# Kernel optimization log

Measured on AMD Instinct MI355X. Metric: run time of the kernel, lower is better.

Reference implementation:

```python
import jax, jax.numpy as jnp
import numpy as np

B, S, E, H, L, D, G, V = 32, 256, 300, 256, 4000, 256, 512, 50000
LIN1, LIN2 = 512, 256  # linear_size


def _glorot(key, shape):
    fan_in, fan_out = shape[-1], shape[-2] if len(shape) > 1 else shape[-1]
    std = np.sqrt(2.0 / (fan_in + fan_out))
    return jax.random.normal(key, shape, dtype=jnp.float32) * std


def setup_inputs() -> dict:
    key = jax.random.key(0)
    ks = jax.random.split(key, 20)
    tokens = jax.random.randint(ks[0], (B, S), 1, V)  # avoid padding_idx=0
    emb_table = jax.random.normal(ks[1], (V, E), dtype=jnp.float32) * 0.1
    emb_table = emb_table.at[0].set(0.0)  # padding row
    # bidirectional LSTM (1 layer), torch gate order i,f,g,o
    w_ih_f = _glorot(ks[2], (4 * H, E));  w_hh_f = _glorot(ks[3], (4 * H, H))
    b_f = jnp.zeros((4 * H,), jnp.float32)
    w_ih_b = _glorot(ks[4], (4 * H, E));  w_hh_b = _glorot(ks[5], (4 * H, H))
    b_b = jnp.zeros((4 * H,), jnp.float32)
    # MLAttention: Linear(2H -> L, bias=False)
    attn_w = _glorot(ks[6], (L, 2 * H))
    # label graph branch
    label_emb = _glorot(ks[7], (L, D))
    adj_raw = (jax.random.uniform(ks[8], (L, L)) < 0.004).astype(jnp.float32)
    adj_raw = adj_raw + jnp.eye(L, dtype=jnp.float32)
    deg = jnp.sum(adj_raw, axis=1, keepdims=True)
    adj = adj_raw / deg  # row-normalized dense adjacency [L, L]
    gcn_w = _glorot(ks[9], (D, G));  gcn_b = jnp.zeros((G,), jnp.float32)
    # MLLinear([2H+G, 512, 256], 1)
    w1 = _glorot(ks[10], (2 * H + G, LIN1));  b1 = jnp.zeros((LIN1,), jnp.float32)
    w2 = _glorot(ks[11], (LIN1, LIN2));       b2 = jnp.zeros((LIN2,), jnp.float32)
    w_out = _glorot(ks[12], (LIN2, 1));       b_out = jnp.zeros((1,), jnp.float32)
    return dict(tokens=tokens, emb_table=emb_table,
                w_ih_f=w_ih_f, w_hh_f=w_hh_f, b_f=b_f,
                w_ih_b=w_ih_b, w_hh_b=w_hh_b, b_b=b_b,
                attn_w=attn_w, label_emb=label_emb, adj=adj,
                gcn_w=gcn_w, gcn_b=gcn_b,
                w1=w1, b1=b1, w2=w2, b2=b2, w_out=w_out, b_out=b_out)


def _lstm_dir(x_gates, w_hh, reverse):
    # x_gates: [B, S, 4H] precomputed input projections (+bias)
    def step(carry, xt):
        h, c = carry
        gates = xt + h @ w_hh.T
        i, f, g, o = jnp.split(gates, 4, axis=-1)
        c = jax.nn.sigmoid(f) * c + jax.nn.sigmoid(i) * jnp.tanh(g)
        h = jax.nn.sigmoid(o) * jnp.tanh(c)
        return (h, c), h
    b = x_gates.shape[0]
    init = (jnp.zeros((b, H), x_gates.dtype), jnp.zeros((b, H), x_gates.dtype))
    _, hs = jax.lax.scan(step, init, jnp.swapaxes(x_gates, 0, 1), reverse=reverse)
    return jnp.swapaxes(hs, 0, 1)  # [B, S, H]


def reference(tokens, emb_table, w_ih_f, w_hh_f, b_f, w_ih_b, w_hh_b, b_b,
              attn_w, label_emb, adj, gcn_w, gcn_b,
              w1, b1, w2, b2, w_out, b_out):
    masks = tokens != 0  # [B, S]
    emb_out = emb_table[tokens]  # [B, S, E]
    # bidirectional LSTM -> [B, S, 2H]
    gates_f = jnp.einsum('bse,ge->bsg', emb_out, w_ih_f) + b_f
    gates_b = jnp.einsum('bse,ge->bsg', emb_out, w_ih_b) + b_b
    rnn_out = jnp.concatenate([_lstm_dir(gates_f, w_hh_f, False),
                               _lstm_dir(gates_b, w_hh_b, True)], axis=-1)
    # MLAttention: per-label attention over sequence
    scores = jnp.einsum('bsh,lh->bls', rnn_out, attn_w)  # [B, L, S]
    scores = jnp.where(masks[:, None, :], scores, jnp.float32(-1e9))
    attn = jax.nn.softmax(scores, axis=-1)
    attn_out = jnp.einsum('bls,bsh->blh', attn, rnn_out)  # [B, L, 2H]
    # GCN over label graph: relu(A @ (X W) + b), single layer [D -> G]
    gcn_out = jax.nn.relu(adj @ (label_emb @ gcn_w) + gcn_b)  # [L, G]
    gcn_out = jnp.broadcast_to(gcn_out[None], (attn_out.shape[0], L, G))
    # concat fusion + MLLinear([2H+G, 512, 256], 1)
    x = jnp.concatenate([attn_out, gcn_out], axis=-1)  # [B, L, 2H+G]
    x = jax.nn.relu(x @ w1 + b1)
    x = jax.nn.relu(x @ w2 + b2)
    out = jnp.squeeze(x @ w_out + b_out, -1)  # [B, L]
    return out
```

## Files before the change

### kernel.cpp

```cpp
#include <hip/hip_runtime.h>
#include <hip/hip_bf16.h>
#include <math.h>


typedef __attribute__((ext_vector_type(8))) short bfrag;
typedef __attribute__((ext_vector_type(4))) float ffrag;

__device__ __forceinline__ ushort f2bf(float x) {
    union { float f; unsigned u; } c; c.f = x;
    const unsigned r = c.u + 0x7fffu + ((c.u >> 16) & 1u);
    return (ushort)(r >> 16);
}
__device__ __forceinline__ float bf2f(ushort h) {
    union { unsigned u; float f; } c; c.u = (unsigned)h << 16;
    return c.f;
}

template<bool BIAS, bool ADDROW, bool RELU, bool OUTF, bool OUTS, bool OUTDOT>
__global__ __launch_bounds__(256) void mgemm_k(
    const ushort* __restrict__ A, const ushort* __restrict__ B,
    float* __restrict__ Cf, ushort* __restrict__ Cs,
    int M, int N, int K, int lda, int ldb, int ldc, int ldcs,
    long abs_, long bbs_, long cbs_, long csbs_,
    const float* __restrict__ bias,
    const float* __restrict__ addrow, int addmod, int ldadd,
    const float* __restrict__ dotw, float* __restrict__ pd)
{
    const int tid = threadIdx.x;
    const int ln = tid & 63;
    const int wv = tid >> 6;
    const int wm = wv >> 1, wn = wv & 1;
    const int n0 = blockIdx.x * 128;
    const int m0 = blockIdx.y * 128;
    const int z = blockIdx.z;
    A += (size_t)z * abs_;
    B += (size_t)z * bbs_;

    __shared__ ushort Ah[128 * 40], Al[128 * 40], Bh[128 * 40], Bl[128 * 40];

    ffrag acc[4][4];
#pragma unroll
    for (int i = 0; i < 4; ++i)
#pragma unroll
        for (int j = 0; j < 4; ++j) acc[i][j] = ffrag{0.f, 0.f, 0.f, 0.f};

    const int sr = tid >> 1;
    const int sk = (tid & 1) * 16;
    const int am = min(m0 + sr, M - 1);
    const int bn = n0 + sr;
    const int fr = ln & 15;
    const int fk = (ln >> 4) * 8;

    const ushort* arow = A + (size_t)am * lda + sk;
    const ushort* brow = B + (size_t)bn * ldb + sk;

    bfrag ah0, ah1, al0, al1, bh0, bh1, bl0, bl1;
    {
        const ushort* ap = arow;
        const ushort* bp = brow;
        ah0 = *(const bfrag*)ap;       ah1 = *(const bfrag*)(ap + 8);
        al0 = *(const bfrag*)(ap + K); al1 = *(const bfrag*)(ap + K + 8);
        bh0 = *(const bfrag*)bp;       bh1 = *(const bfrag*)(bp + 8);
        bl0 = *(const bfrag*)(bp + K); bl1 = *(const bfrag*)(bp + K + 8);
    }

    for (int k0 = 0; k0 < K; k0 += 32) {
        __syncthreads();
        *(bfrag*)&Ah[sr * 40 + sk] = ah0;  *(bfrag*)&Ah[sr * 40 + sk + 8] = ah1;
        *(bfrag*)&Al[sr * 40 + sk] = al0;  *(bfrag*)&Al[sr * 40 + sk + 8] = al1;
        *(bfrag*)&Bh[sr * 40 + sk] = bh0;  *(bfrag*)&Bh[sr * 40 + sk + 8] = bh1;
        *(bfrag*)&Bl[sr * 40 + sk] = bl0;  *(bfrag*)&Bl[sr * 40 + sk + 8] = bl1;
        __syncthreads();
        if (k0 + 32 < K) {
            const ushort* ap = arow + k0 + 32;
            const ushort* bp = brow + k0 + 32;
            ah0 = *(const bfrag*)ap;       ah1 = *(const bfrag*)(ap + 8);
            al0 = *(const bfrag*)(ap + K); al1 = *(const bfrag*)(ap + K + 8);
            bh0 = *(const bfrag*)bp;       bh1 = *(const bfrag*)(bp + 8);
            bl0 = *(const bfrag*)(bp + K); bl1 = *(const bfrag*)(bp + K + 8);
        }
        bfrag afh[4], afl[4];
#pragma unroll
        for (int i = 0; i < 4; ++i) {
            const int ar = (wm * 64 + i * 16 + fr) * 40 + fk;
            afh[i] = *(const bfrag*)&Ah[ar];
            afl[i] = *(const bfrag*)&Al[ar];
        }
#pragma unroll
        for (int j = 0; j < 4; ++j) {
            const int br = (wn * 64 + j * 16 + fr) * 40 + fk;
            const bfrag bfh = *(const bfrag*)&Bh[br];
            const bfrag bfl = *(const bfrag*)&Bl[br];
#pragma unroll
            for (int i = 0; i < 4; ++i) {
                acc[i][j] = __builtin_amdgcn_mfma_f32_16x16x32_bf16(afh[i], bfh, acc[i][j], 0, 0, 0);
                acc[i][j] = __builtin_amdgcn_mfma_f32_16x16x32_bf16(afh[i], bfl, acc[i][j], 0, 0, 0);
                acc[i][j] = __builtin_amdgcn_mfma_f32_16x16x32_bf16(afl[i], bfh, acc[i][j], 0, 0, 0);
            }
        }
    }

    if (OUTDOT) {
        float wv4[4], bv4[4];
#pragma unroll
        for (int j = 0; j < 4; ++j) {
            const int gn = n0 + wn * 64 + j * 16 + fr;
            wv4[j] = dotw[gn];
            bv4[j] = BIAS ? bias[gn] : 0.f;
        }
        float rsum[16];
#pragma unroll
        for (int i = 0; i < 4; ++i) {
#pragma unroll
            for (int rg = 0; rg < 4; ++rg) {
                const int gm = m0 + wm * 64 + i * 16 + (ln >> 4) * 4 + rg;
                float p = 0.f;
                if (gm < M) {
#pragma unroll
                    for (int j = 0; j < 4; ++j) {
                        float v = acc[i][j][rg] + bv4[j];
                        if (RELU) v = fmaxf(v, 0.f);
                        p = fmaf(v, wv4[j], p);
                    }
                }
                rsum[i * 4 + rg] = p;
            }
        }
#pragma unroll
        for (int t = 0; t < 16; ++t) {
            rsum[t] += __shfl_xor(rsum[t], 1);
            rsum[t] += __shfl_xor(rsum[t], 2);
            rsum[t] += __shfl_xor(rsum[t], 4);
            rsum[t] += __shfl_xor(rsum[t], 8);
        }
        float* pdls = (float*)Ah;
        __syncthreads();
        if (wn == 0 && fr == 0) {
#pragma unroll
            for (int i = 0; i < 4; ++i)
#pragma unroll
                for (int rg = 0; rg < 4; ++rg)
                    pdls[wm * 64 + i * 16 + (ln >> 4) * 4 + rg] = rsum[i * 4 + rg];
        }
        __syncthreads();
        if (wn == 1 && fr == 0) {
#pragma unroll
            for (int i = 0; i < 4; ++i)
#pragma unroll
                for (int rg = 0; rg < 4; ++rg) {
                    const int lr = wm * 64 + i * 16 + (ln >> 4) * 4 + rg;
                    const int gm = m0 + lr;
                    if (gm < M) pd[(size_t)blockIdx.x * M + gm] = pdls[lr] + rsum[i * 4 + rg];
                }
        }
        return;
    }

#pragma unroll
    for (int i = 0; i < 4; ++i) {
#pragma unroll
        for (int rg = 0; rg < 4; ++rg) {
            const int gm = m0 + wm * 64 + i * 16 + (ln >> 4) * 4 + rg;
            if (gm >= M) continue;
            const float* addp = ADDROW ? (addrow + (size_t)(gm % addmod) * ldadd) : nullptr;
#pragma unroll
            for (int j = 0; j < 4; ++j) {
                const int gn = n0 + wn * 64 + j * 16 + fr;
                float v = acc[i][j][rg];
                if (BIAS) v += bias[gn];
                if (ADDROW) v += addp[gn];
                if (RELU) v = fmaxf(v, 0.f);
                if (OUTF) Cf[(size_t)z * cbs_ + (size_t)gm * ldc + gn] = v;
                if (OUTS) {
                    const ushort h = f2bf(v);
                    const ushort l = f2bf(v - bf2f(h));
                    ushort* cp = Cs + (size_t)z * csbs_ + (size_t)gm * ldcs;
                    cp[gn] = h;
                    cp[N + gn] = l;
                }
            }
        }
    }
}

__global__ void outsum_k(const float* __restrict__ pd, const float* __restrict__ b_out,
                         float* __restrict__ outp, int M, int b0)
{
    const int r = blockIdx.x * 256 + threadIdx.x;
    if (r >= M) return;
    const int bb = r / 4000, l = r - bb * 4000;
    outp[(size_t)(b0 + bb) * 4000 + l] = (pd[r] + pd[(size_t)M + r]) + b_out[0];
}

__global__ void gsplit_k(const float* __restrict__ src, const int* __restrict__ tok,
                         ushort* __restrict__ outp, int K, int Kpad)
{
    const int r = blockIdx.x;
    const float* s = src + (size_t)(tok ? tok[r] : r) * K;
    ushort* o = outp + (size_t)r * 2 * Kpad;
    for (int k = threadIdx.x; k < Kpad; k += blockDim.x) {
        const float x = (k < K) ? s[k] : 0.f;
        const ushort h = f2bf(x);
        const ushort l = f2bf(x - bf2f(h));
        o[k] = h;
        o[Kpad + k] = l;
    }
}

__global__ void split_k(const float* __restrict__ in, ushort* __restrict__ outp,
                        int rows, int K)
{
    const int i = blockIdx.x * 256 + threadIdx.x;
    if (i >= rows * K) return;
    const int r = i / K, k = i - r * K;
    const float x = in[i];
    const ushort h = f2bf(x);
    const ushort l = f2bf(x - bf2f(h));
    ushort* o = outp + (size_t)r * 2 * K;
    o[k] = h;
    o[K + k] = l;
}

__global__ __launch_bounds__(256) void tsplit_k(
    const float* __restrict__ in, ushort* __restrict__ outp,
    int R, int C, int ldin, long ibs, long obs)
{
    __shared__ float t[64][65];
    const int c0 = blockIdx.x * 64, r0 = blockIdx.y * 64;
    in   += (size_t)blockIdx.z * ibs;
    outp += (size_t)blockIdx.z * obs;
    const int tx = threadIdx.x & 15, ty = threadIdx.x >> 4;
#pragma unroll
    for (int i = 0; i < 4; ++i) {
        const int r = ty * 4 + i;
        const float4 v = *(const float4*)&in[(size_t)(r0 + r) * ldin + c0 + tx * 4];
        t[tx * 4 + 0][r] = v.x;
        t[tx * 4 + 1][r] = v.y;
        t[tx * 4 + 2][r] = v.z;
        t[tx * 4 + 3][r] = v.w;
    }
    __syncthreads();
    const int R2 = 2 * R;
#pragma unroll
    for (int i = 0; i < 4; ++i) {
        const int c = ty * 4 + i;
        ushort h[4], l[4];
#pragma unroll
        for (int k2 = 0; k2 < 4; ++k2) {
            const float x = t[c][tx * 4 + k2];
            h[k2] = f2bf(x);
            l[k2] = f2bf(x - bf2f(h[k2]));
        }
        uint2 hw, lw;
        hw.x = (unsigned)h[0] | ((unsigned)h[1] << 16);
        hw.y = (unsigned)h[2] | ((unsigned)h[3] << 16);
        lw.x = (unsigned)l[0] | ((unsigned)l[1] << 16);
        lw.y = (unsigned)l[2] | ((unsigned)l[3] << 16);
        *(uint2*)&outp[(size_t)(c0 + c) * R2 + r0 + tx * 4] = hw;
        *(uint2*)&outp[(size_t)(c0 + c) * R2 + R + r0 + tx * 4] = lw;
    }
}

__global__ __launch_bounds__(1024) void lstm_reg_k(
    const float* __restrict__ gxf, const float* __restrict__ gxb,
    const float* __restrict__ whf, const float* __restrict__ whb,
    float* __restrict__ rnn, float* hbuf, int* stamp)
{
    const int p = blockIdx.x;
    const int q = blockIdx.y;
    const int b = p >> 1, dir = p & 1;
    const float* xg = dir ? gxb : gxf;
    const float* W  = dir ? whb : whf;
    const int tid = threadIdx.x;
    const int wv = tid >> 6, lane = tid & 63;
    const int ul = lane >> 4;
    const int ks = (lane >> 2) & 3;
    const int gt = lane & 3;
    const int u  = wv * 4 + ul;
    const int grow = gt * 256 + q * 64 + u;

    float4 w[16];
    {
        const float4* wp = (const float4*)(W + (size_t)grow * 256 + ks * 64);
#pragma unroll
        for (int i = 0; i < 16; ++i) w[i] = wp[i];
    }

    __shared__ float h_lds[4 * 68];
    __shared__ float xg_lds[320];

    float* hb0 = hbuf + (size_t)p * 256;
    float* hb1 = hbuf + (size_t)(64 + p) * 256;
    int* sp = stamp + p * 16;

    const size_t xgb = (size_t)b * 256;
    const int g2 = (tid >> 6) * 256 + q * 64 + (tid & 63);
    float c = 0.f;
    float xg_cur = 0.f;
    if (tid < 256) xg_cur = xg[(xgb + (dir ? 255 : 0)) * 1024 + g2];

    for (int st = 0; st < 256; ++st) {
        const int ts = dir ? 255 - st : st;
        if (st > 0 && tid == 0) {
            while (true) {
                int s0 = __hip_atomic_load(&sp[0], __ATOMIC_RELAXED, __HIP_MEMORY_SCOPE_AGENT);
                int s1 = __hip_atomic_load(&sp[1], __ATOMIC_RELAXED, __HIP_MEMORY_SCOPE_AGENT);
                int s2 = __hip_atomic_load(&sp[2], __ATOMIC_RELAXED, __HIP_MEMORY_SCOPE_AGENT);
                int s3 = __hip_atomic_load(&sp[3], __ATOMIC_RELAXED, __HIP_MEMORY_SCOPE_AGENT);
                if (min(min(s0, s1), min(s2, s3)) >= st) break;
            }
        }
        __syncthreads();
        if (tid < 256) {
            float hv = 0.f;
            if (st > 0) {
                const float* src = (st & 1) ? hb0 : hb1;
                hv = __hip_atomic_load(&src[tid], __ATOMIC_RELAXED, __HIP_MEMORY_SCOPE_AGENT);
            }
            h_lds[(tid >> 6) * 68 + (tid & 63)] = hv;
            xg_lds[(tid & 63) * 5 + (tid >> 6)] = xg_cur;
        }
        __syncthreads();
        float acc = 0.f;
        {
            const float4* hp = (const float4*)&h_lds[ks * 68];
#pragma unroll
            for (int i = 0; i < 16; ++i) {
                const float4 hv = hp[i];
                acc = fmaf(w[i].x, hv.x, acc);
                acc = fmaf(w[i].y, hv.y, acc);
                acc = fmaf(w[i].z, hv.z, acc);
                acc = fmaf(w[i].w, hv.w, acc);
            }
        }
        acc += __shfl_xor(acc, 4);
        acc += __shfl_xor(acc, 8);
        const float g = acc + xg_lds[u * 5 + gt];
        const float t1 = __shfl_xor(g, 1);
        const float t2 = __shfl_xor(g, 2);
        const float t3 = __shfl_xor(t1, 2);
        const float g0 = (gt == 0) ? g : (gt == 1) ? t1 : (gt == 2) ? t2 : t3;
        const float g1 = (gt == 1) ? g : (gt == 0) ? t1 : (gt == 3) ? t2 : t3;
        const float g2v = (gt == 2) ? g : (gt == 3) ? t1 : (gt == 0) ? t2 : t3;
        const float g3v = (gt == 3) ? g : (gt == 2) ? t1 : (gt == 1) ? t2 : t3;
        const float si = 1.f / (1.f + __expf(-g0));
        const float sf = 1.f / (1.f + __expf(-g1));
        const float so = 1.f / (1.f + __expf(-g3v));
        const float tg = 1.f - 2.f / (__expf(2.f * g2v) + 1.f);
        c = sf * c + si * tg;
        const float tc = 1.f - 2.f / (__expf(2.f * c) + 1.f);
        const float hn = so * tc;
        if ((lane & 15) == 0) {
            float* dst = (st & 1) ? hb1 : hb0;
            __hip_atomic_store(&dst[q * 64 + u], hn, __ATOMIC_RELAXED, __HIP_MEMORY_SCOPE_AGENT);
            rnn[(xgb + ts) * 512 + (size_t)dir * 256 + q * 64 + u] = hn;
        }
        __syncthreads();
        if (tid == 0) {
            __hip_atomic_store(&sp[q], st + 1, __ATOMIC_RELAXED, __HIP_MEMORY_SCOPE_AGENT);
        }
        if (tid < 256 && st < 255) {
            const int tsn = dir ? 254 - st : st + 1;
            xg_cur = xg[(xgb + tsn) * 1024 + g2];
        }
    }
}

__global__ void init_cnt_k(int* stamp) {
    const int i = blockIdx.x * blockDim.x + threadIdx.x;
    if (i < 1024) stamp[i] = 0;
}

__global__ __launch_bounds__(256) void softmax_split_k(
    float* __restrict__ sc, const int* __restrict__ tokens, int b0)
{
    const int bb = blockIdx.y;
    const int l  = blockIdx.x * 4 + (threadIdx.x >> 6);
    const int lane = threadIdx.x & 63;
    float* row = sc + ((size_t)bb * 4000 + l) * 256;
    const int* tk = tokens + (size_t)(b0 + bb) * 256;
    float4 v = *(const float4*)&row[lane * 4];
    const int4 tv = *(const int4*)&tk[lane * 4];
    if (tv.x == 0) v.x = -1e9f;
    if (tv.y == 0) v.y = -1e9f;
    if (tv.z == 0) v.z = -1e9f;
    if (tv.w == 0) v.w = -1e9f;
    float mx = fmaxf(fmaxf(v.x, v.y), fmaxf(v.z, v.w));
    for (int o = 32; o > 0; o >>= 1) mx = fmaxf(mx, __shfl_xor(mx, o));
    v.x = __expf(v.x - mx); v.y = __expf(v.y - mx);
    v.z = __expf(v.z - mx); v.w = __expf(v.w - mx);
    float s = v.x + v.y + v.z + v.w;
    for (int o = 32; o > 0; o >>= 1) s += __shfl_xor(s, o);
    const float inv = 1.f / s;
    const float p0 = v.x * inv, p1 = v.y * inv, p2 = v.z * inv, p3 = v.w * inv;
    const ushort h0 = f2bf(p0), h1 = f2bf(p1), h2 = f2bf(p2), h3 = f2bf(p3);
    const ushort l0 = f2bf(p0 - bf2f(h0)), l1 = f2bf(p1 - bf2f(h1));
    const ushort l2 = f2bf(p2 - bf2f(h2)), l3 = f2bf(p3 - bf2f(h3));
    ushort* orow = (ushort*)row;
    uint2 hw, lw;
    hw.x = (unsigned)h0 | ((unsigned)h1 << 16);
    hw.y = (unsigned)h2 | ((unsigned)h3 << 16);
    lw.x = (unsigned)l0 | ((unsigned)l1 << 16);
    lw.y = (unsigned)l2 | ((unsigned)l3 << 16);
    *(uint2*)&orow[lane * 4] = hw;
    *(uint2*)&orow[256 + lane * 4] = lw;
}

__global__ __launch_bounds__(256) void spmm_k(
    const float* __restrict__ adj, const float* __restrict__ tmp,
    const float* __restrict__ bias, float* __restrict__ outp)
{
    const int l = blockIdx.x;
    __shared__ int   idxs[4][256];
    __shared__ float vals[4][256];
    __shared__ int   cnts[4];
    const int t = threadIdx.x;
    const int w = t >> 6, lane = t & 63;
    const float* arow = adj + (size_t)l * 4000;
    int cnt = 0;
    for (int r = 0; r < 16; ++r) {
        const int o = r * 64 + lane;
        const int j = w * 1000 + o;
        const float a = (o < 1000) ? arow[j] : 0.f;
        const unsigned long long mk = __ballot(a != 0.f);
        if (a != 0.f) {
            const int pos = cnt + __popcll(mk & ((1ull << lane) - 1ull));
            if (pos < 256) { idxs[w][pos] = j; vals[w][pos] = a; }
        }
        cnt += __popcll(mk);
    }
    if (lane == 0) cnts[w] = min(cnt, 256);
    __syncthreads();
    const int c0 = t * 2;
    float a0 = 0.f, a1 = 0.f;
    for (int ww = 0; ww < 4; ++ww) {
        const int n = cnts[ww];
        for (int e = 0; e < n; ++e) {
            const float a = vals[ww][e];
            const float2 tv = *(const float2*)&tmp[(size_t)idxs[ww][e] * 512 + c0];
            a0 = fmaf(a, tv.x, a0);
            a1 = fmaf(a, tv.y, a1);
        }
    }
    float2 res;
    res.x = fmaxf(a0 + bias[c0], 0.f);
    res.y = fmaxf(a1 + bias[c0 + 1], 0.f);
    *(float2*)&outp[(size_t)l * 512 + c0] = res;
}

extern "C" void kernel_launch(void* const* d_in, const int* in_sizes, int n_in,
                              void* d_out, int out_size, void* d_ws, size_t ws_size,
                              hipStream_t stream)
{
    const int*   tokens    = (const int*)  d_in[0];
    const float* emb       = (const float*)d_in[1];
    const float* w_ih_f    = (const float*)d_in[2];
    const float* w_hh_f    = (const float*)d_in[3];
    const float* b_f       = (const float*)d_in[4];
    const float* w_ih_b    = (const float*)d_in[5];
    const float* w_hh_b    = (const float*)d_in[6];
    const float* b_b       = (const float*)d_in[7];
    const float* attn_w    = (const float*)d_in[8];
    const float* label_emb = (const float*)d_in[9];
    const float* adj       = (const float*)d_in[10];
    const float* gcn_w     = (const float*)d_in[11];
    const float* gcn_b     = (const float*)d_in[12];
    const float* w1        = (const float*)d_in[13];
    const float* b1        = (const float*)d_in[14];
    const float* w2        = (const float*)d_in[15];
    const float* b2        = (const float*)d_in[16];
    const float* w_out     = (const float*)d_in[17];
    const float* b_out     = (const float*)d_in[18];
    float* outp = (float*)d_out;
    float* wsf  = (float*)d_ws;

    const size_t off_gf  = 0;
    const size_t off_gb  = 8388608;
    const size_t off_rnn = 16777216;
    const size_t off_tmp = 20971520;
    const size_t off_go  = 23019520;
    const size_t off_ctr = 25067520;
    const size_t base_end = 27115520;
    const size_t S_sz = 10829824;
    const size_t have = ws_size / 4;
    int NB = 1; size_t offS = off_gf, offC = off_gf + S_sz;
    {
        const int tiers[6] = {32, 16, 8, 4, 2, 0};
        bool found = false;
        for (int t = 0; tiers[t]; ++t) {
            if (have >= base_end + S_sz + (size_t)tiers[t] * 5120000) {
                NB = tiers[t]; offS = base_end; offC = base_end + S_sz; found = true; break;
            }
        }
        if (!found && have >= base_end + S_sz) { NB = 2; offS = base_end; offC = off_gf; }
    }

    float* gates_f = wsf + off_gf;
    float* gates_b = wsf + off_gb;
    float* rnn     = wsf + off_rnn;
    float* gcn_tmp = wsf + off_tmp;
    float* gcn_out = wsf + off_go;
    float* contrib = wsf + off_ctr;
    float* hbuf    = wsf + off_tmp;
    int*   stamp   = (int*)(wsf + off_tmp + 32768);

    const size_t off_esp = (offS == off_gf) ? off_rnn : offS;
    ushort* esplit  = (ushort*)(wsf + off_esp);
    ushort* wsplitf = esplit + (size_t)8192 * 640;
    ushort* wsplitb = wsplitf + (size_t)1024 * 640;

    ushort* attn_ws16 = (ushort*)(wsf + offS);
    ushort* w1t16     = (ushort*)(wsf + offS + 2048000);
    ushort* w2t16     = (ushort*)(wsf + offS + 2310144);
    ushort* rnn_nt16  = (ushort*)(wsf + offS + 2441216);
    ushort* rnnT16    = (ushort*)(wsf + offS + 6635520);

    float*  scoresb = wsf + offC;
    ushort* attn16  = (ushort*)(wsf + offC + (size_t)NB * 1024000);
    ushort* x116    = (ushort*)(wsf + offC + (size_t)NB * 1024000 + (size_t)NB * 2048000);
    float*  pd      = scoresb;

    ushort* le16   = (ushort*)(wsf + offC);
    ushort* gw16   = le16 + (size_t)4000 * 512;
    ushort* go16   = gw16 + (size_t)512 * 512;
    ushort* w1b16  = go16 + (size_t)4000 * 1024;

    init_cnt_k<<<4, 256, 0, stream>>>(stamp);

    gsplit_k<<<8192, 256, 0, stream>>>(emb, tokens, esplit, 300, 320);
    gsplit_k<<<1024, 256, 0, stream>>>(w_ih_f, nullptr, wsplitf, 300, 320);
    gsplit_k<<<1024, 256, 0, stream>>>(w_ih_b, nullptr, wsplitb, 300, 320);
    mgemm_k<true, false, false, true, false, false><<<dim3(8, 64, 1), 256, 0, stream>>>(
        esplit, wsplitf, gates_f, nullptr,
        8192, 1024, 320, 640, 640, 1024, 0,
        0L, 0L, 0L, 0L, b_f, nullptr, 1, 0, nullptr, nullptr);
    mgemm_k<true, false, false, true, false, false><<<dim3(8, 64, 1), 256, 0, stream>>>(
        esplit, wsplitb, gates_b, nullptr,
        8192, 1024, 320, 640, 640, 1024, 0,
        0L, 0L, 0L, 0L, b_b, nullptr, 1, 0, nullptr, nullptr);

    lstm_reg_k<<<dim3(64, 4), 1024, 0, stream>>>(
        gates_f, gates_b, w_hh_f, w_hh_b, rnn, hbuf, stamp);

    split_k<<<16384, 256, 0, stream>>>(rnn, rnn_nt16, 8192, 512);
    tsplit_k<<<dim3(8, 4, 32), 256, 0, stream>>>(rnn, rnnT16, 256, 512, 512, 131072, 262144);
    split_k<<<8000, 256, 0, stream>>>(attn_w, attn_ws16, 4000, 512);
    tsplit_k<<<dim3(8, 8, 1), 256, 0, stream>>>(w1, w1t16, 512, 512, 512, 0, 0);
    tsplit_k<<<dim3(4, 8, 1), 256, 0, stream>>>(w2, w2t16, 512, 256, 256, 0, 0);

    split_k<<<4000, 256, 0, stream>>>(label_emb, le16, 4000, 256);
    tsplit_k<<<dim3(8, 4, 1), 256, 0, stream>>>(gcn_w, gw16, 256, 512, 512, 0, 0);
    mgemm_k<false, false, false, true, false, false><<<dim3(4, 32, 1), 256, 0, stream>>>(
        le16, gw16, gcn_tmp, nullptr,
        4000, 512, 256, 512, 512, 512, 0,
        0L, 0L, 0L, 0L, nullptr, nullptr, 1, 0, nullptr, nullptr);
    spmm_k<<<dim3(4000), 256, 0, stream>>>(adj, gcn_tmp, gcn_b, gcn_out);
    split_k<<<8000, 256, 0, stream>>>(gcn_out, go16, 4000, 512);
    tsplit_k<<<dim3(8, 8, 1), 256, 0, stream>>>(w1 + (size_t)512 * 512, w1b16, 512, 512, 512, 0, 0);
    mgemm_k<true, false, false, true, false, false><<<dim3(4, 32, 1), 256, 0, stream>>>(
        go16, w1b16, contrib, nullptr,
        4000, 512, 512, 1024, 1024, 512, 0,
        0L, 0L, 0L, 0L, b1, nullptr, 1, 0, nullptr, nullptr);

    for (int b0 = 0; b0 < 32; b0 += NB) {
        const int nb = (32 - b0 < NB) ? (32 - b0) : NB;
        mgemm_k<false, false, false, true, false, false><<<dim3(2, 32, nb), 256, 0, stream>>>(
            attn_ws16, rnn_nt16 + (size_t)b0 * 262144, scoresb, nullptr,
            4000, 256, 512, 1024, 1024, 256, 0,
            0L, 262144L, 1024000L, 0L, nullptr, nullptr, 1, 0, nullptr, nullptr);
        softmax_split_k<<<dim3(1000, nb), 256, 0, stream>>>(scoresb, tokens, b0);
        mgemm_k<false, false, false, false, true, false><<<dim3(4, 32, nb), 256, 0, stream>>>(
            (const ushort*)scoresb, rnnT16 + (size_t)b0 * 262144, nullptr, attn16,
            4000, 512, 256, 512, 512, 0, 1024,
            2048000L, 262144L, 0L, 4096000L, nullptr, nullptr, 1, 0, nullptr, nullptr);
        mgemm_k<false, true, true, false, true, false><<<dim3(4, (nb * 4000 + 127) / 128, 1), 256, 0, stream>>>(
            attn16, w1t16, nullptr, x116,
            nb * 4000, 512, 512, 1024, 1024, 0, 1024,
            0L, 0L, 0L, 0L, nullptr, contrib, 4000, 512, nullptr, nullptr);
        mgemm_k<true, false, true, false, false, true><<<dim3(2, (nb * 4000 + 127) / 128, 1), 256, 0, stream>>>(
            x116, w2t16, nullptr, nullptr,
            nb * 4000, 256, 512, 1024, 1024, 0, 0,
            0L, 0L, 0L, 0L, b2, nullptr, 1, 0, w_out, pd);
        outsum_k<<<(nb * 4000 + 255) / 256, 256, 0, stream>>>(pd, b_out, outp, nb * 4000, b0);
    }
}
```

Baseline: 1.757 ms.

## Load GEMM tiles directly into LDS with swizzled layout instead of register staging

Replaces the register-staged global loads followed by LDS stores with direct global-to-LDS loads (global_load_lds, 16 bytes per lane). Padded 40-element rows become unpadded 32-element rows with an XOR swizzle to avoid LDS bank conflicts. This drops VGPR staging and the separate ds_write instructions. It also drops the register prefetch of the next tile, so global load latency is no longer overlapped with the MFMA work of the previous iteration.

After: 1.800 ms. 1.02x slower.

```diff
diff --git a/kernel.cpp b/kernel.cpp
--- a/kernel.cpp
+++ b/kernel.cpp
@@ -14,6 +14,12 @@
 __device__ __forceinline__ float bf2f(ushort h) {
     union { unsigned u; float f; } c; c.u = (unsigned)h << 16;
     return c.f;
+}
+
+__device__ __forceinline__ void gload16(const ushort* g, ushort* l) {
+    __builtin_amdgcn_global_load_lds(
+        (const __attribute__((address_space(1))) void*)g,
+        (__attribute__((address_space(3))) void*)l, 16, 0, 0);
 }
 
 template<bool BIAS, bool ADDROW, bool RELU, bool OUTF, bool OUTS, bool OUTDOT>
@@ -36,7 +42,7 @@
     A += (size_t)z * abs_;
     B += (size_t)z * bbs_;
 
-    __shared__ ushort Ah[128 * 40], Al[128 * 40], Bh[128 * 40], Bl[128 * 40];
+    __shared__ ushort Ah[128 * 32], Al[128 * 32], Bh[128 * 32], Bl[128 * 32];
 
     ffrag acc[4][4];
 #pragma unroll
@@ -44,51 +50,41 @@
 #pragma unroll
         for (int j = 0; j < 4; ++j) acc[i][j] = ffrag{0.f, 0.f, 0.f, 0.f};
 
-    const int sr = tid >> 1;
-    const int sk = (tid & 1) * 16;
-    const int am = min(m0 + sr, M - 1);
-    const int bn = n0 + sr;
+    const int srow = ln >> 2;
+    const int csrc = (ln & 3) ^ ((ln >> 3) & 3);
+    const int arow0 = min(m0 + wv * 16 + srow, M - 1);
+    const int arow1 = min(m0 + 64 + wv * 16 + srow, M - 1);
+    const int brow0 = n0 + wv * 16 + srow;
+    const int brow1 = n0 + 64 + wv * 16 + srow;
+    const ushort* agp0 = A + (size_t)arow0 * lda + csrc * 8;
+    const ushort* agp1 = A + (size_t)arow1 * lda + csrc * 8;
+    const ushort* bgp0 = B + (size_t)brow0 * ldb + csrc * 8;
+    const ushort* bgp1 = B + (size_t)brow1 * ldb + csrc * 8;
+    ushort* lAh0 = &Ah[wv * 512];  ushort* lAh1 = &Ah[2048 + wv * 512];
+    ushort* lAl0 = &Al[wv * 512];  ushort* lAl1 = &Al[2048 + wv * 512];
+    ushort* lBh0 = &Bh[wv * 512];  ushort* lBh1 = &Bh[2048 + wv * 512];
+    ushort* lBl0 = &Bl[wv * 512];  ushort* lBl1 = &Bl[2048 + wv * 512];
+
     const int fr = ln & 15;
-    const int fk = (ln >> 4) * 8;
-
-    const ushort* arow = A + (size_t)am * lda + sk;
-    const ushort* brow = B + (size_t)bn * ldb + sk;
-
-    bfrag ah0, ah1, al0, al1, bh0, bh1, bl0, bl1;
-    {
-        const ushort* ap = arow;
-        const ushort* bp = brow;
-        ah0 = *(const bfrag*)ap;       ah1 = *(const bfrag*)(ap + 8);
-        al0 = *(const bfrag*)(ap + K); al1 = *(const bfrag*)(ap + K + 8);
-        bh0 = *(const bfrag*)bp;       bh1 = *(const bfrag*)(bp + 8);
-        bl0 = *(const bfrag*)(bp + K); bl1 = *(const bfrag*)(bp + K + 8);
-    }
+    const int sw = ((ln >> 4) ^ ((fr >> 1) & 3)) * 8;
 
     for (int k0 = 0; k0 < K; k0 += 32) {
         __syncthreads();
-        *(bfrag*)&Ah[sr * 40 + sk] = ah0;  *(bfrag*)&Ah[sr * 40 + sk + 8] = ah1;
-        *(bfrag*)&Al[sr * 40 + sk] = al0;  *(bfrag*)&Al[sr * 40 + sk + 8] = al1;
-        *(bfrag*)&Bh[sr * 40 + sk] = bh0;  *(bfrag*)&Bh[sr * 40 + sk + 8] = bh1;
-        *(bfrag*)&Bl[sr * 40 + sk] = bl0;  *(bfrag*)&Bl[sr * 40 + sk + 8] = bl1;
-        __syncthreads();
-        if (k0 + 32 < K) {
-            const ushort* ap = arow + k0 + 32;
-            const ushort* bp = brow + k0 + 32;
-            ah0 = *(const bfrag*)ap;       ah1 = *(const bfrag*)(ap + 8);
-            al0 = *(const bfrag*)(ap + K); al1 = *(const bfrag*)(ap + K + 8);
-            bh0 = *(const bfrag*)bp;       bh1 = *(const bfrag*)(bp + 8);
-            bl0 = *(const bfrag*)(bp + K); bl1 = *(const bfrag*)(bp + K + 8);
-        }
+        gload16(agp0 + k0, lAh0);      gload16(agp1 + k0, lAh1);
+        gload16(agp0 + k0 + K, lAl0);  gload16(agp1 + k0 + K, lAl1);
+        gload16(bgp0 + k0, lBh0);      gload16(bgp1 + k0, lBh1);
+        gload16(bgp0 + k0 + K, lBl0);  gload16(bgp1 + k0 + K, lBl1);
+        __syncthreads();
         bfrag afh[4], afl[4];
 #pragma unroll
         for (int i = 0; i < 4; ++i) {
-            const int ar = (wm * 64 + i * 16 + fr) * 40 + fk;
+            const int ar = (wm * 64 + i * 16 + fr) * 32 + sw;
             afh[i] = *(const bfrag*)&Ah[ar];
             afl[i] = *(const bfrag*)&Al[ar];
         }
 #pragma unroll
         for (int j = 0; j < 4; ++j) {
-            const int br = (wn * 64 + j * 16 + fr) * 40 + fk;
+            const int br = (wn * 64 + j * 16 + fr) * 32 + sw;
             const bfrag bfh = *(const bfrag*)&Bh[br];
             const bfrag bfl = *(const bfrag*)&Bl[br];
 #pragma unroll
```
